# Kernel tuning notes

Measured on AMD Instinct MI355X. Metric: run time of the kernel, lower is better.

The kernel has to match this reference:

```python
import jax, jax.numpy as jnp
import numpy as np

N = 100000      # nodes
E = 1600000     # edges
F_IN, H1, H2, H3, F_OUT = 64, 128, 128, 64, 8


def _lin(key, fan_in, fan_out):
    return jax.random.normal(key, (fan_in, fan_out), jnp.float32) / np.sqrt(fan_in).astype(np.float32)


def setup_inputs() -> dict:
    key = jax.random.key(0)
    ks = jax.random.split(key, 16)
    x = jax.random.normal(ks[0], (N, F_IN), jnp.float32)
    edge_index = jax.random.randint(ks[1], (2, E), 0, N, dtype=jnp.int64)
    return {
        "x": x,
        "edge_index": edge_index,
        "eps1": jnp.zeros((), jnp.float32),
        "eps2": jnp.zeros((), jnp.float32),
        "eps3": jnp.zeros((), jnp.float32),
        "W1a": _lin(ks[2], F_IN, H1), "b1a": jnp.zeros((H1,), jnp.float32),
        "W1b": _lin(ks[3], H1, H1),   "b1b": jnp.zeros((H1,), jnp.float32),
        "W2a": _lin(ks[4], H1, H2),   "b2a": jnp.zeros((H2,), jnp.float32),
        "W2b": _lin(ks[5], H2, H2),   "b2b": jnp.zeros((H2,), jnp.float32),
        "W3a": _lin(ks[6], H2, H3),   "b3a": jnp.zeros((H3,), jnp.float32),
        "W3b": _lin(ks[7], H3, H3),   "b3b": jnp.zeros((H3,), jnp.float32),
        "Wfc": _lin(ks[8], H3, F_OUT), "bfc": jnp.zeros((F_OUT,), jnp.float32),
    }


def _gin_conv(x, src, dst, eps, Wa, ba, Wb, bb):
    # out_i = MLP((1+eps) * x_i + sum_{j in N(i)} x_j)
    agg = jax.ops.segment_sum(x[src], dst, num_segments=N)  # scatter-add over edges
    h = (1.0 + eps) * x + agg
    return jax.nn.relu(h @ Wa + ba) @ Wb + bb


def reference(x, edge_index, eps1, eps2, eps3,
              W1a, b1a, W1b, b1b,
              W2a, b2a, W2b, b2b,
              W3a, b3a, W3b, b3b,
              Wfc, bfc):
    src, dst = edge_index[0], edge_index[1]
    x = jax.nn.relu(_gin_conv(x, src, dst, eps1, W1a, b1a, W1b, b1b))
    x = jax.nn.relu(_gin_conv(x, src, dst, eps2, W2a, b2a, W2b, b2b))
    x = jax.nn.relu(_gin_conv(x, src, dst, eps3, W3a, b3a, W3b, b3b))
    emb = jax.lax.stop_gradient(x)  # x.clone().detach()
    out = x @ Wfc + bfc
    return out, emb
```

## Files before the change

kernel.cpp:

```cpp
#include <hip/hip_runtime.h>
#include <hip/hip_bf16.h>
#include <stdint.h>

typedef unsigned short ushort_t;
typedef __attribute__((ext_vector_type(8))) short short8;
typedef __attribute__((ext_vector_type(4))) float floatx4;

__device__ __forceinline__ float bf2f(unsigned short u){
  union { unsigned int i; float f; } v; v.i = ((unsigned int)u) << 16; return v.f;
}
__device__ __forceinline__ unsigned short f2bf(float f){
  union { float f; unsigned int i; } v; v.f = f;
  unsigned int r = v.i + 0x7FFFu + ((v.i >> 16) & 1u);
  return (unsigned short)(r >> 16);
}
__device__ __forceinline__ unsigned int pack2(unsigned short lo, unsigned short hi){
  return ((unsigned int)hi << 16) | (unsigned int)lo;
}
__device__ __forceinline__ float bflo(unsigned int v){
  union { unsigned int u; float f; } c; c.u = v << 16; return c.f;
}
__device__ __forceinline__ float bfhi(unsigned int v){
  union { unsigned int u; float f; } c; c.u = v & 0xffff0000u; return c.f;
}


__global__ __launch_bounds__(256)
void k_prep(const unsigned int* __restrict__ w, int* __restrict__ ghist, int E, int N, int nbB,
            const float2* __restrict__ xin, unsigned int* __restrict__ xb, int total2, int tobfB,
            const float* __restrict__ W1a, const float* __restrict__ W1b, const float* __restrict__ W2a,
            const float* __restrict__ W2b, const float* __restrict__ W3a, const float* __restrict__ W3b,
            const float* __restrict__ Wfc, ushort_t* __restrict__ wout)
{
  int b = blockIdx.x, t = threadIdx.x;
  if (b < nbB){
    __shared__ int h[256];
    __shared__ unsigned int dred[4];
    h[t] = 0;
    int base = b*4096 + t;
    unsigned int acc = 0;
    #pragma unroll
    for (int i=0;i<16;++i){
      int e = base + i*256;
      if (e < E) acc |= w[2*e+1];
    }
    #pragma unroll
    for (int o=32;o>=1;o>>=1) acc |= __shfl_xor(acc, o);
    if ((t&63)==0) dred[t>>6] = acc;
    __syncthreads();
    int m = (dred[0]|dred[1]|dred[2]|dred[3]) != 0;
    #pragma unroll
    for (int i=0;i<16;++i){
      int e = base + i*256;
      if (e < E){
        int d = m ? (int)w[(size_t)E + e] : (int)w[2*((size_t)E + e)];
        if ((unsigned)d < (unsigned)N) atomicAdd(&h[d>>9], 1);
      }
    }
    __syncthreads();
    if (h[t]) atomicAdd(&ghist[t], h[t]);
  } else if (b < nbB + tobfB){
    int i = (b - nbB)*256 + t;
    if (i < total2){
      float2 v = xin[i];
      xb[i] = pack2(f2bf(v.x), f2bf(v.y));
    }
  } else {
    int id = (b - nbB - tobfB)*256 + t;
    const float* src; int K, M, base2, local;
    if      (id <  8192){ src=W1a; K=64;  M=128; base2=0;     local=id; }
    else if (id < 24576){ src=W1b; K=128; M=128; base2=8192;  local=id-8192; }
    else if (id < 40960){ src=W2a; K=128; M=128; base2=24576; local=id-24576; }
    else if (id < 57344){ src=W2b; K=128; M=128; base2=40960; local=id-40960; }
    else if (id < 65536){ src=W3a; K=128; M=64;  base2=57344; local=id-57344; }
    else if (id < 69632){ src=W3b; K=64;  M=64;  base2=65536; local=id-65536; }
    else if (id < 70656){ src=Wfc; K=64;  M=16;  base2=69632; local=id-69632; }
    else return;
    int k = local / M, nn = local - k*M;
    float val;
    if (src == Wfc) val = (nn<8) ? Wfc[k*8+nn] : 0.0f;
    else            val = src[k*M+nn];
    int idx = (((nn>>4)*(K/32) + (k>>5))*4 + ((k>>3)&3))*128 + (nn&15)*8 + (k&7);
    wout[base2+idx] = f2bf(val);
  }
}


__global__ __launch_bounds__(256) void k_bscan(const int* __restrict__ ghist, int* __restrict__ bbase,
                                               int* __restrict__ gcur, int NB){
  __shared__ int sv[256];
  int t = threadIdx.x;
  int v = (t < NB) ? ghist[t] : 0;
  sv[t] = v; __syncthreads();
  for (int o=1;o<256;o<<=1){
    int xv = (t>=o)? sv[t-o] : 0;
    __syncthreads();
    sv[t] += xv;
    __syncthreads();
  }
  int excl = sv[t] - v;
  if (t < NB){ bbase[t] = excl; gcur[t] = excl; }
  if (t == NB-1) bbase[NB] = excl + v;
}

__global__ __launch_bounds__(256) void k_bin(const unsigned int* __restrict__ w,
                                             int* __restrict__ gcur, int2* __restrict__ pairs,
                                             int E, int N, int NB){
  __shared__ int h[256];
  __shared__ int cur[256];
  __shared__ unsigned int dred[4];
  int t = threadIdx.x;
  h[t] = 0;
  int base = blockIdx.x*4096 + t;
  unsigned int acc = 0;
  #pragma unroll
  for (int i=0;i<16;++i){
    int e = base + i*256;
    if (e < E) acc |= w[2*e+1];
  }
  #pragma unroll
  for (int o=32;o>=1;o>>=1) acc |= __shfl_xor(acc, o);
  if ((t&63)==0) dred[t>>6] = acc;
  __syncthreads();
  int m = (dred[0]|dred[1]|dred[2]|dred[3]) != 0;
  int d[16], s[16];
  #pragma unroll
  for (int i=0;i<16;++i){
    int e = base + i*256;
    d[i] = -1; s[i] = 0;
    if (e < E){
      if (m){ s[i] = (int)w[e];           d[i] = (int)w[(size_t)E + e]; }
      else  { s[i] = (int)w[2*(size_t)e]; d[i] = (int)w[2*((size_t)E + e)]; }
      if ((unsigned)d[i] >= (unsigned)N || (unsigned)s[i] >= (unsigned)N) d[i] = -1;
    }
  }
  #pragma unroll
  for (int i=0;i<16;++i)
    if (d[i] >= 0) atomicAdd(&h[d[i]>>9], 1);
  __syncthreads();
  if (t < NB && h[t]) cur[t] = atomicAdd(&gcur[t], h[t]);
  __syncthreads();
  #pragma unroll
  for (int i=0;i<16;++i){
    if (d[i] >= 0){
      int p = atomicAdd(&cur[d[i]>>9], 1);
      pairs[p] = make_int2(d[i], s[i]);
    }
  }
}

__global__ __launch_bounds__(256) void k_bcsr(const int2* __restrict__ pairs, const int* __restrict__ bbase,
                                              int* __restrict__ offs, int* __restrict__ csr, int N, int NB){
  __shared__ int cnt[512];
  __shared__ int wsum[4];
  int b = blockIdx.x, t = threadIdx.x, lane = t&63, wv = t>>6;
  int lo = bbase[b], hi = bbase[b+1];
  int node0 = b << 9;
  cnt[t] = 0; cnt[t+256] = 0;
  __syncthreads();
  for (int i = lo+t; i < hi; i += 256){
    int2 p = pairs[i];
    atomicAdd(&cnt[p.x - node0], 1);
  }
  __syncthreads();
  int v0 = cnt[2*t], v1 = cnt[2*t+1], tot = v0+v1;
  int s = tot;
  #pragma unroll
  for (int o=1;o<64;o<<=1){ int xv = __shfl_up(s,o); if (lane>=o) s += xv; }
  if (lane==63) wsum[wv] = s;
  __syncthreads();
  int basev = 0;
  for (int j=0;j<wv;++j) basev += wsum[j];
  int excl = basev + s - tot;
  int e0 = lo + excl, e1 = lo + excl + v0;
  cnt[2*t] = e0; cnt[2*t+1] = e1;
  int n0 = node0 + 2*t, n1 = node0 + 2*t + 1;
  if (n0 < N) offs[n0] = e0;
  if (n1 < N) offs[n1] = e1;
  if (b == NB-1 && t == 255) offs[N] = hi;
  __syncthreads();
  for (int i = lo+t; i < hi; i += 256){
    int2 p = pairs[i];
    int pos = atomicAdd(&cnt[p.x - node0], 1);
    csr[pos] = p.y;
  }
}


template<int F>
__global__ __launch_bounds__(256) void k_gatherx(const uint2* __restrict__ xr, const int* __restrict__ offs,
                                                 const int* __restrict__ csr, const float* __restrict__ epsp,
                                                 uint2* __restrict__ hr, int n){
  constexpr int G = F/4;
  constexpr int NPW = 64/(2*G);
  int gt = blockIdx.x*256 + threadIdx.x;
  int wv = gt >> 6, lane = gt & 63;
  int grp  = lane / (2*G);
  int half = (lane / G) & 1;
  int f    = lane % G;
  int node = wv*NPW + grp;
  if (node >= n) return;
  const size_t row = (size_t)node*G;
  uint2 sv = xr[row + f];
  float e1s = 1.0f + epsp[0];
  float a0, a1, a2, a3;
  if (half == 0){
    a0 = e1s*bflo(sv.x); a1 = e1s*bfhi(sv.x);
    a2 = e1s*bflo(sv.y); a3 = e1s*bfhi(sv.y);
  } else { a0 = a1 = a2 = a3 = 0.f; }
  int u0 = offs[node], u1 = offs[node+1];
  int u = u0;
#define ACC4(v) { a0 += bflo((v).x); a1 += bfhi((v).x); a2 += bflo((v).y); a3 += bfhi((v).y); }
  for (; u+15 < u1; u += 16){
    int s0 = csr[u    + half], s1 = csr[u+2  + half], s2 = csr[u+4  + half], s3 = csr[u+6  + half];
    int s4 = csr[u+8  + half], s5 = csr[u+10 + half], s6 = csr[u+12 + half], s7 = csr[u+14 + half];
    uint2 v0 = xr[(size_t)s0*G + f];
    uint2 v1 = xr[(size_t)s1*G + f];
    uint2 v2 = xr[(size_t)s2*G + f];
    uint2 v3 = xr[(size_t)s3*G + f];
    uint2 v4 = xr[(size_t)s4*G + f];
    uint2 v5 = xr[(size_t)s5*G + f];
    uint2 v6 = xr[(size_t)s6*G + f];
    uint2 v7 = xr[(size_t)s7*G + f];
    ACC4(v0) ACC4(v1) ACC4(v2) ACC4(v3) ACC4(v4) ACC4(v5) ACC4(v6) ACC4(v7)
  }
  for (; u+7 < u1; u += 8){
    int s0 = csr[u + half], s1 = csr[u+2 + half], s2 = csr[u+4 + half], s3 = csr[u+6 + half];
    uint2 v0 = xr[(size_t)s0*G + f];
    uint2 v1 = xr[(size_t)s1*G + f];
    uint2 v2 = xr[(size_t)s2*G + f];
    uint2 v3 = xr[(size_t)s3*G + f];
    ACC4(v0) ACC4(v1) ACC4(v2) ACC4(v3)
  }
  for (; u+1 < u1; u += 2){
    int s = csr[u + half];
    uint2 v = xr[(size_t)s*G + f];
    ACC4(v)
  }
  if (u < u1 && half == 0){
    int s = csr[u];
    uint2 v = xr[(size_t)s*G + f];
    ACC4(v)
  }
#undef ACC4
  a0 += __shfl_xor(a0, G);
  a1 += __shfl_xor(a1, G);
  a2 += __shfl_xor(a2, G);
  a3 += __shfl_xor(a3, G);
  if (half == 0){
    uint2 o2;
    o2.x = pack2(f2bf(a0), f2bf(a1));
    o2.y = pack2(f2bf(a2), f2bf(a3));
    hr[row + f] = o2;
  }
}


template<int F, int M1, int M2, bool LAST>
__global__ __launch_bounds__(256)
void k_mlp(const ushort_t* __restrict__ h,
           const ushort_t* __restrict__ wp1, const float* __restrict__ b1,
           const ushort_t* __restrict__ wp2, const float* __restrict__ b2,
           ushort_t* __restrict__ xout,
           float* __restrict__ embp,
           const ushort_t* __restrict__ wpfc, const float* __restrict__ bfc,
           float* __restrict__ outp, int n)
{
  constexpr int NT1 = M1/16, NT2 = M2/16, KC1 = F/32, KC2 = M1/32;
  __shared__ short sC1[4*(M1/8)*136];
  __shared__ short sX3[LAST ? (4*8*136) : 1];
  int tid = threadIdx.x, lane = tid&63, w = tid>>6;
  int m16 = lane&15, quad = lane>>4;
  int row0 = blockIdx.x*64 + w*16;
  size_t arow = (size_t)(row0 + m16);

  floatx4 acc[NT1];
  #pragma unroll
  for (int i=0;i<NT1;++i) acc[i] = (floatx4){0.f,0.f,0.f,0.f};
  #pragma unroll
  for (int kc=0; kc<KC1; ++kc){
    short8 a = *(const short8*)(h + arow*F + kc*32 + quad*8);
    #pragma unroll
    for (int nt=0; nt<NT1; ++nt){
      short8 b = *(const short8*)(wp1 + (size_t)((nt*KC1+kc)*64 + lane)*8);
      acc[nt] = __builtin_amdgcn_mfma_f32_16x16x32_bf16(a, b, acc[nt], 0, 0, 0);
    }
  }
  #pragma unroll
  for (int nt=0; nt<NT1; ++nt){
    int c = nt*16 + m16;
    float bias = b1[c];
    #pragma unroll
    for (int r=0;r<4;++r){
      float v = fmaxf(acc[nt][r] + bias, 0.f);
      int mm = quad*4 + r;
      sC1[(w*(M1/8) + (c>>3))*136 + mm*8 + (c&7)] = (short)f2bf(v);
    }
  }
  __syncthreads();

  floatx4 acc2[NT2];
  #pragma unroll
  for (int i=0;i<NT2;++i) acc2[i] = (floatx4){0.f,0.f,0.f,0.f};
  #pragma unroll
  for (int kc=0; kc<KC2; ++kc){
    short8 a = *(const short8*)&sC1[(w*(M1/8) + kc*4 + quad)*136 + m16*8];
    #pragma unroll
    for (int nt=0; nt<NT2; ++nt){
      short8 b = *(const short8*)(wp2 + (size_t)((nt*KC2+kc)*64 + lane)*8);
      acc2[nt] = __builtin_amdgcn_mfma_f32_16x16x32_bf16(a, b, acc2[nt], 0, 0, 0);
    }
  }
  #pragma unroll
  for (int nt=0; nt<NT2; ++nt){
    int c = nt*16 + m16;
    float bias = b2[c];
    #pragma unroll
    for (int r=0;r<4;++r){
      float v = fmaxf(acc2[nt][r] + bias, 0.f);
      int mm = quad*4 + r;
      int row = row0 + mm;
      if constexpr (!LAST){
        if (row < n) xout[(size_t)row*M2 + c] = f2bf(v);
      } else {
        if (row < n) embp[(size_t)row*64 + c] = v;
        sX3[(w*8 + (c>>3))*136 + mm*8 + (c&7)] = (short)f2bf(v);
      }
    }
  }

  if constexpr (LAST){
    __syncthreads();
    floatx4 accf = (floatx4){0.f,0.f,0.f,0.f};
    #pragma unroll
    for (int kc=0; kc<2; ++kc){
      short8 a = *(const short8*)&sX3[(w*8 + kc*4 + quad)*136 + m16*8];
      short8 b = *(const short8*)(wpfc + (size_t)(kc*64 + lane)*8);
      accf = __builtin_amdgcn_mfma_f32_16x16x32_bf16(a, b, accf, 0, 0, 0);
    }
    if (m16 < 8){
      float bias = bfc[m16];
      #pragma unroll
      for (int r=0;r<4;++r){
        int row = row0 + quad*4 + r;
        if (row < n) outp[(size_t)row*8 + m16] = accf[r] + bias;
      }
    }
  }
}


extern "C" void kernel_launch(void* const* d_in, const int* in_sizes, int n_in,
                              void* d_out, int out_size, void* d_ws, size_t ws_size,
                              hipStream_t stream)
{
  const int N = in_sizes[0] / 64;
  const int E = in_sizes[1] / 2;
  const int NB = (N + 511) / 512;
  const float*        x    = (const float*)d_in[0];
  const unsigned int* ew   = (const unsigned int*)d_in[1];
  const float* eps1 = (const float*)d_in[2];
  const float* eps2 = (const float*)d_in[3];
  const float* eps3 = (const float*)d_in[4];
  const float* W1a  = (const float*)d_in[5];
  const float* b1a  = (const float*)d_in[6];
  const float* W1b  = (const float*)d_in[7];
  const float* b1b  = (const float*)d_in[8];
  const float* W2a  = (const float*)d_in[9];
  const float* b2a  = (const float*)d_in[10];
  const float* W2b  = (const float*)d_in[11];
  const float* b2b  = (const float*)d_in[12];
  const float* W3a  = (const float*)d_in[13];
  const float* b3a  = (const float*)d_in[14];
  const float* W3b  = (const float*)d_in[15];
  const float* b3b  = (const float*)d_in[16];
  const float* Wfc  = (const float*)d_in[17];
  const float* bfc  = (const float*)d_in[18];

  float* outp = (float*)d_out;
  float* emb  = outp + (size_t)N*8;

  const int Npad = ((N + 63)/64)*64;

  char* ws = (char*)d_ws;
  size_t o = 0;
  auto alloc = [&](size_t bytes)->char* {
    char* p = ws + o;
    o = (o + bytes + 255) & ~(size_t)255;
    return p;
  };
  int*      ghist = (int*)alloc(256*4);
  int*      bbase = (int*)alloc(257*4);
  int*      gcur  = (int*)alloc(256*4);
  int*      offs  = (int*)alloc((size_t)(N+1)*4);
  int2*     pairs = (int2*)alloc((size_t)E*8);
  int*      csr   = (int*)alloc((size_t)E*4);
  ushort_t* wperm = (ushort_t*)alloc(70656ull*2);
  ushort_t* xb    = (ushort_t*)alloc((size_t)Npad*64*2);
  ushort_t* hbuf  = (ushort_t*)alloc((size_t)Npad*128*2);
  ushort_t* x1    = (ushort_t*)alloc((size_t)Npad*128*2);

  hipMemsetAsync(ghist, 0, 256*4, stream);
  const int nbB   = (E + 4095)/4096;
  const int tobfB = (N*32 + 255)/256;
  const int permB = 70656/256;
  k_prep<<<nbB + tobfB + permB, 256, 0, stream>>>(ew, ghist, E, N, nbB,
                                                  (const float2*)x, (unsigned int*)xb, N*32, tobfB,
                                                  W1a, W1b, W2a, W2b, W3a, W3b, Wfc, wperm);
  k_bscan<<<1, 256, 0, stream>>>(ghist, bbase, gcur, NB);
  k_bin<<<nbB, 256, 0, stream>>>(ew, gcur, pairs, E, N, NB);
  k_bcsr<<<NB, 256, 0, stream>>>(pairs, bbase, offs, csr, N, NB);

  k_gatherx<64><<<(((N+1)/2)+3)/4, 256, 0, stream>>>((const uint2*)xb, offs, csr, eps1,
                                                     (uint2*)hbuf, N);
  k_mlp<64,128,128,false><<<Npad/64, 256, 0, stream>>>(hbuf, wperm+0, b1a, wperm+8192, b1b,
                                                       x1, nullptr, nullptr, nullptr, nullptr, N);
  k_gatherx<128><<<(N+3)/4, 256, 0, stream>>>((const uint2*)x1, offs, csr, eps2,
                                              (uint2*)hbuf, N);
  k_mlp<128,128,128,false><<<Npad/64, 256, 0, stream>>>(hbuf, wperm+24576, b2a, wperm+40960, b2b,
                                                        x1, nullptr, nullptr, nullptr, nullptr, N);
  k_gatherx<128><<<(N+3)/4, 256, 0, stream>>>((const uint2*)x1, offs, csr, eps3,
                                              (uint2*)hbuf, N);
  k_mlp<128,64,64,true><<<Npad/64, 256, 0, stream>>>(hbuf, wperm+57344, b3a, wperm+65536, b3b,
                                                     nullptr, emb, wperm+69632, bfc, outp, N);
}
```

Measured before the change: 411.4 us.

## Widen gather to 16-byte loads with wave-cooperative CSR index broadcast

The neighbour-aggregation kernel now gives each lane 16-byte (8 bf16) loads and splits every node across four edge-parallel lane groups instead of two. The lanes of a node load CSR indices together, one per lane, and share them with shuffles, so each thread no longer loads the same index values itself. Padding to the chunk size reads a zeroed dummy row, which requires extra allocation and a memset for that row. This reduces index-load and instruction overhead per edge, at the cost of wasted loads on low-degree nodes and extra shuffles.

```diff
diff --git a/kernel.cpp b/kernel.cpp
--- a/kernel.cpp
+++ b/kernel.cpp
@@ -188,70 +188,70 @@
 
 
 template<int F>
-__global__ __launch_bounds__(256) void k_gatherx(const uint2* __restrict__ xr, const int* __restrict__ offs,
+__global__ __launch_bounds__(256) void k_gatherx(const uint4* __restrict__ xr, const int* __restrict__ offs,
                                                  const int* __restrict__ csr, const float* __restrict__ epsp,
-                                                 uint2* __restrict__ hr, int n){
-  constexpr int G = F/4;
-  constexpr int NPW = 64/(2*G);
+                                                 uint4* __restrict__ hr, int n, int nzrow){
+  constexpr int RS  = F/8;
+  constexpr int LPN = 4*RS;
+  constexpr int NPW = 64/LPN;
+  constexpr int CH  = LPN;
   int gt = blockIdx.x*256 + threadIdx.x;
   int wv = gt >> 6, lane = gt & 63;
-  int grp  = lane / (2*G);
-  int half = (lane / G) & 1;
-  int f    = lane % G;
+  int grp = lane / LPN;
+  int lin = lane % LPN;
+  int q   = lin / RS;
+  int f   = lin % RS;
   int node = wv*NPW + grp;
   if (node >= n) return;
-  const size_t row = (size_t)node*G;
-  uint2 sv = xr[row + f];
+  const size_t row = (size_t)node*RS;
   float e1s = 1.0f + epsp[0];
-  float a0, a1, a2, a3;
-  if (half == 0){
-    a0 = e1s*bflo(sv.x); a1 = e1s*bfhi(sv.x);
-    a2 = e1s*bflo(sv.y); a3 = e1s*bfhi(sv.y);
-  } else { a0 = a1 = a2 = a3 = 0.f; }
+  float a[8];
+  if (q == 0){
+    uint4 sv = xr[row + f];
+    a[0]=e1s*bflo(sv.x); a[1]=e1s*bfhi(sv.x);
+    a[2]=e1s*bflo(sv.y); a[3]=e1s*bfhi(sv.y);
+    a[4]=e1s*bflo(sv.z); a[5]=e1s*bfhi(sv.z);
+    a[6]=e1s*bflo(sv.w); a[7]=e1s*bfhi(sv.w);
+  } else {
+    #pragma unroll
+    for (int i=0;i<8;++i) a[i]=0.f;
+  }
   int u0 = offs[node], u1 = offs[node+1];
-  int u = u0;
-#define ACC4(v) { a0 += bflo((v).x); a1 += bfhi((v).x); a2 += bflo((v).y); a3 += bfhi((v).y); }
-  for (; u+15 < u1; u += 16){
-    int s0 = csr[u    + half], s1 = csr[u+2  + half], s2 = csr[u+4  + half], s3 = csr[u+6  + half];
-    int s4 = csr[u+8  + half], s5 = csr[u+10 + half], s6 = csr[u+12 + half], s7 = csr[u+14 + half];
-    uint2 v0 = xr[(size_t)s0*G + f];
-    uint2 v1 = xr[(size_t)s1*G + f];
-    uint2 v2 = xr[(size_t)s2*G + f];
-    uint2 v3 = xr[(size_t)s3*G + f];
-    uint2 v4 = xr[(size_t)s4*G + f];
-    uint2 v5 = xr[(size_t)s5*G + f];
-    uint2 v6 = xr[(size_t)s6*G + f];
-    uint2 v7 = xr[(size_t)s7*G + f];
-    ACC4(v0) ACC4(v1) ACC4(v2) ACC4(v3) ACC4(v4) ACC4(v5) ACC4(v6) ACC4(v7)
-  }
-  for (; u+7 < u1; u += 8){
-    int s0 = csr[u + half], s1 = csr[u+2 + half], s2 = csr[u+4 + half], s3 = csr[u+6 + half];
-    uint2 v0 = xr[(size_t)s0*G + f];
-    uint2 v1 = xr[(size_t)s1*G + f];
-    uint2 v2 = xr[(size_t)s2*G + f];
-    uint2 v3 = xr[(size_t)s3*G + f];
-    ACC4(v0) ACC4(v1) ACC4(v2) ACC4(v3)
-  }
-  for (; u+1 < u1; u += 2){
-    int s = csr[u + half];
-    uint2 v = xr[(size_t)s*G + f];
-    ACC4(v)
-  }
-  if (u < u1 && half == 0){
-    int s = csr[u];
-    uint2 v = xr[(size_t)s*G + f];
-    ACC4(v)
-  }
-#undef ACC4
-  a0 += __shfl_xor(a0, G);
-  a1 += __shfl_xor(a1, G);
-  a2 += __shfl_xor(a2, G);
-  a3 += __shfl_xor(a3, G);
-  if (half == 0){
-    uint2 o2;
-    o2.x = pack2(f2bf(a0), f2bf(a1));
-    o2.y = pack2(f2bf(a2), f2bf(a3));
-    hr[row + f] = o2;
+  int deg = u1 - u0;
+#define ACC8(v) { a[0]+=bflo((v).x); a[1]+=bfhi((v).x); a[2]+=bflo((v).y); a[3]+=bfhi((v).y); \
+                  a[4]+=bflo((v).z); a[5]+=bfhi((v).z); a[6]+=bflo((v).w); a[7]+=bfhi((v).w); }
+  for (int c0 = 0; c0 < deg; c0 += CH){
+    int rem = deg - c0;
+    int cv = nzrow;
+    if (lin < rem) cv = csr[u0 + c0 + lin];
+    int nk = rem < CH ? rem : CH;
+    int ng = (nk + 15) >> 4;
+    for (int g = 0; g < ng; ++g){
+      int b = grp*LPN + g*16 + q;
+      int s0 = __shfl(cv, b);
+      int s1 = __shfl(cv, b+4);
+      int s2 = __shfl(cv, b+8);
+      int s3 = __shfl(cv, b+12);
+      uint4 v0 = xr[(size_t)s0*RS + f];
+      uint4 v1 = xr[(size_t)s1*RS + f];
+      uint4 v2 = xr[(size_t)s2*RS + f];
+      uint4 v3 = xr[(size_t)s3*RS + f];
+      ACC8(v0) ACC8(v1) ACC8(v2) ACC8(v3)
+    }
+  }
+#undef ACC8
+  #pragma unroll
+  for (int i=0;i<8;++i){
+    a[i] += __shfl_xor(a[i], RS);
+    a[i] += __shfl_xor(a[i], 2*RS);
+  }
+  if (q == 0){
+    uint4 o;
+    o.x = pack2(f2bf(a[0]), f2bf(a[1]));
+    o.y = pack2(f2bf(a[2]), f2bf(a[3]));
+    o.z = pack2(f2bf(a[4]), f2bf(a[5]));
+    o.w = pack2(f2bf(a[6]), f2bf(a[7]));
+    hr[row + f] = o;
   }
 }
 
@@ -396,11 +396,13 @@
   int2*     pairs = (int2*)alloc((size_t)E*8);
   int*      csr   = (int*)alloc((size_t)E*4);
   ushort_t* wperm = (ushort_t*)alloc(70656ull*2);
-  ushort_t* xb    = (ushort_t*)alloc((size_t)Npad*64*2);
+  ushort_t* xb    = (ushort_t*)alloc(((size_t)Npad + 64)*64*2);
   ushort_t* hbuf  = (ushort_t*)alloc((size_t)Npad*128*2);
-  ushort_t* x1    = (ushort_t*)alloc((size_t)Npad*128*2);
+  ushort_t* x1    = (ushort_t*)alloc(((size_t)Npad + 64)*128*2);
 
   hipMemsetAsync(ghist, 0, 256*4, stream);
+  hipMemsetAsync(xb + (size_t)N*64, 0, 64*2, stream);
+  hipMemsetAsync(x1 + (size_t)N*128, 0, 128*2, stream);
   const int nbB   = (E + 4095)/4096;
   const int tobfB = (N*32 + 255)/256;
   const int permB = 70656/256;
@@ -411,16 +413,16 @@
   k_bin<<<nbB, 256, 0, stream>>>(ew, gcur, pairs, E, N, NB);
   k_bcsr<<<NB, 256, 0, stream>>>(pairs, bbase, offs, csr, N, NB);
 
-  k_gatherx<64><<<(((N+1)/2)+3)/4, 256, 0, stream>>>((const uint2*)xb, offs, csr, eps1,
-                                                     (uint2*)hbuf, N);
+  k_gatherx<64><<<(N+7)/8, 256, 0, stream>>>((const uint4*)xb, offs, csr, eps1,
+                                             (uint4*)hbuf, N, N);
   k_mlp<64,128,128,false><<<Npad/64, 256, 0, stream>>>(hbuf, wperm+0, b1a, wperm+8192, b1b,
                                                        x1, nullptr, nullptr, nullptr, nullptr, N);
-  k_gatherx<128><<<(N+3)/4, 256, 0, stream>>>((const uint2*)x1, offs, csr, eps2,
-                                              (uint2*)hbuf, N);
+  k_gatherx<128><<<(N+3)/4, 256, 0, stream>>>((const uint4*)x1, offs, csr, eps2,
+                                              (uint4*)hbuf, N, N);
   k_mlp<128,128,128,false><<<Npad/64, 256, 0, stream>>>(hbuf, wperm+24576, b2a, wperm+40960, b2b,
                                                         x1, nullptr, nullptr, nullptr, nullptr, N);
-  k_gatherx<128><<<(N+3)/4, 256, 0, stream>>>((const uint2*)x1, offs, csr, eps3,
-                                              (uint2*)hbuf, N);
+  k_gatherx<128><<<(N+3)/4, 256, 0, stream>>>((const uint4*)x1, offs, csr, eps3,
+                                              (uint4*)hbuf, N, N);
   k_mlp<128,64,64,true><<<Npad/64, 256, 0, stream>>>(hbuf, wperm+57344, b3a, wperm+65536, b3b,
                                                      nullptr, emb, wperm+69632, bfc, outp, N);
 }
```

After: 393.3 us. 1.05x faster.
